# Performance work log

Measured on AMD Instinct MI355X. Metric: run time of the kernel, lower is better.

## Reference

```python
import jax, jax.numpy as jnp
import numpy as np

B, IN, OUT, K = 2048, 1024, 1024, 20


def setup_inputs() -> dict:
    key = jax.random.key(0)
    k1, k2 = jax.random.split(key)
    x = jax.random.normal(k1, (B, IN), dtype=jnp.float32)
    # per-output, per-input spline coefficients: (out_features, in_features, num_knots)
    W = jax.random.normal(k2, (OUT, IN, K), dtype=jnp.float32) * 0.1
    # evenly spaced knot grid on [-2, 2] (linspace)
    knots = jnp.linspace(-2.0, 2.0, K, dtype=jnp.float32)
    return {"x": x, "W": W, "knots": knots}


def reference(x, W, knots):
    # RBF spline basis shared across all output features (this is the fusion
    # the original per-output Python loop misses):
    # basis[b, i, k] = exp(-0.5 * ((x[b, i] - knots[k]) / h)^2)
    h = knots[1] - knots[0]  # uniform knot spacing -> RBF bandwidth
    basis = jnp.exp(-0.5 * jnp.square((x[:, :, None] - knots) / h))  # (B, IN, K)
    # Each SplineLayer o computes sum_{i,k} W[o,i,k] * basis[b,i,k]; the
    # KANBlock concatenates the OUT scalars -> a single einsum.
    return jnp.einsum("bik,oik->bo", basis, W)  # (B, OUT)
```

## Files before the change

### kernel.cpp

```cpp
#include <hip/hip_runtime.h>

#define B_DIM 2048
#define IN_DIM 1024
#define OUT_DIM 1024
#define K_KNOTS 20
#define KR (IN_DIM * K_KNOTS)
#define TM 128
#define TN 128
#define BK 64
#define OUT_ELEMS (B_DIM * OUT_DIM)

#define NB_PAIRS (B_DIM * IN_DIM * K_KNOTS / 2)
#define NB_BASIS_BLK (NB_PAIRS / 256)
#define NW4 (OUT_DIM * KR / 8)
#define NB_W_BLK (NW4 / 256)

typedef __bf16 bf16x8 __attribute__((ext_vector_type(8)));
typedef float  f32x4  __attribute__((ext_vector_type(4)));

__device__ __forceinline__ unsigned short f2bf(float f) {
    unsigned int u = __float_as_uint(f);
    unsigned int r = u + 0x7fffu + ((u >> 16) & 1u);
    return (unsigned short)(r >> 16);
}

__device__ __forceinline__ unsigned int pack2(float lo, float hi) {
    return (unsigned int)f2bf(lo) | ((unsigned int)f2bf(hi) << 16);
}

__device__ __forceinline__ void async_load16(const void* g, void* l) {
    __builtin_amdgcn_global_load_lds(
        (const __attribute__((address_space(1))) void*)g,
        (__attribute__((address_space(3))) void*)l,
        16, 0, 0);
}

__global__ void zero_out_kernel(float* out) {
    int idx = (blockIdx.x * 256 + threadIdx.x) * 4;
    float4 z = {0.f, 0.f, 0.f, 0.f};
    *(float4*)(out + idx) = z;
}

__global__ void prep_kernel(const float* __restrict__ x,
                            const float4* __restrict__ Wsrc,
                            const float* __restrict__ knots,
                            unsigned int* __restrict__ basis_out,
                            uint4* __restrict__ w_out) {
    if (blockIdx.x < NB_BASIS_BLK) {
        unsigned int n = blockIdx.x * 256 + threadIdx.x;
        unsigned int p  = n % 10u;
        unsigned int bi = n / 10u;
        float xv   = x[bi];
        float invh = 1.0f / (knots[1] - knots[0]);
        float t0 = knots[2 * p], t1 = knots[2 * p + 1];
        float d0 = (xv - t0) * invh;
        float d1 = (xv - t1) * invh;
        float v0 = __expf(-0.5f * d0 * d0);
        float v1 = __expf(-0.5f * d1 * d1);
        basis_out[n] = pack2(v0, v1);
    } else {
        unsigned int t = (blockIdx.x - NB_BASIS_BLK) * 256 + threadIdx.x;
        float4 a = Wsrc[2 * t];
        float4 b = Wsrc[2 * t + 1];
        uint4 o;
        o.x = pack2(a.x, a.y);
        o.y = pack2(a.z, a.w);
        o.z = pack2(b.x, b.y);
        o.w = pack2(b.z, b.w);
        w_out[t] = o;
    }
}

template <int KS, bool ATOMIC>
__global__ void __launch_bounds__(256)
kan_gemm(const unsigned short* __restrict__ Ab,
         const unsigned short* __restrict__ Bb,
         float* __restrict__ out) {
    __shared__ __align__(16) unsigned short As[TM * BK];
    __shared__ __align__(16) unsigned short Bs[TN * BK];

    const int KPB = KR / KS;
    const int tid  = threadIdx.x;
    const int wave = tid >> 6;
    const int lane = tid & 63;
    const int wm = wave & 1;
    const int wn = wave >> 1;
    const int m0 = blockIdx.x * TM;
    const int n0 = blockIdx.y * TN;
    const int k0 = blockIdx.z * KPB;

    const int srow = lane >> 3;
    const int scol = ((lane & 7) ^ srow) * 8;

    f32x4 acc[4][4];
#pragma unroll
    for (int i = 0; i < 4; ++i)
#pragma unroll
        for (int j = 0; j < 4; ++j) acc[i][j] = (f32x4){0.f, 0.f, 0.f, 0.f};

    for (int kt = 0; kt < KPB; kt += BK) {
        const int kb = k0 + kt;
        __syncthreads();
#pragma unroll
        for (int c = 0; c < 4; ++c) {
            const int chunk = wave * 4 + c;
            const int r = chunk * 8 + srow;
            async_load16(Ab + (size_t)(m0 + r) * KR + kb + scol, &As[chunk * 512]);
            async_load16(Bb + (size_t)(n0 + r) * KR + kb + scol, &Bs[chunk * 512]);
        }
        __syncthreads();

        const int quad = lane >> 4;
        const int r15  = lane & 15;
        const int r7   = lane & 7;
#pragma unroll
        for (int s = 0; s < 2; ++s) {
            const int cg = s * 4 + quad;
            const int xo = (cg ^ r7) * 8;
            bf16x8 af[4], bfv[4];
#pragma unroll
            for (int i = 0; i < 4; ++i) {
                af[i]  = *(const bf16x8*)&As[(wm * 64 + i * 16 + r15) * BK + xo];
                bfv[i] = *(const bf16x8*)&Bs[(wn * 64 + i * 16 + r15) * BK + xo];
            }
#pragma unroll
            for (int i = 0; i < 4; ++i)
#pragma unroll
                for (int j = 0; j < 4; ++j)
                    acc[i][j] = __builtin_amdgcn_mfma_f32_16x16x32_bf16(
                        af[i], bfv[j], acc[i][j], 0, 0, 0);
        }
    }

    float* dst = ATOMIC ? out : out + (size_t)blockIdx.z * OUT_ELEMS;
    const int quad = lane >> 4;
    const int col  = lane & 15;
#pragma unroll
    for (int i = 0; i < 4; ++i)
#pragma unroll
        for (int j = 0; j < 4; ++j)
#pragma unroll
            for (int r = 0; r < 4; ++r) {
                const int row = m0 + wm * 64 + i * 16 + quad * 4 + r;
                const int c   = n0 + wn * 64 + j * 16 + col;
                if (ATOMIC)
                    atomicAdd(&dst[(size_t)row * OUT_DIM + c], acc[i][j][r]);
                else
                    dst[(size_t)row * OUT_DIM + c] = acc[i][j][r];
            }
}

template <int KS>
__global__ void kan_reduce(const float* __restrict__ part, float* __restrict__ out) {
    const int idx = (blockIdx.x * 256 + threadIdx.x) * 4;
    f32x4 s = *(const f32x4*)(part + idx);
#pragma unroll
    for (int z = 1; z < KS; ++z)
        s += *(const f32x4*)(part + (size_t)z * OUT_ELEMS + idx);
    *(f32x4*)(out + idx) = s;
}

__global__ void kan_fallback(const float* __restrict__ x,
                             const float* __restrict__ W,
                             const float* __restrict__ knots,
                             float* __restrict__ out) {
    __shared__ float basis[256 * K_KNOTS];
    const int b = blockIdx.x;
    const int o = blockIdx.y * blockDim.x + threadIdx.x;
    const float invh = 1.0f / (knots[1] - knots[0]);
    const float* w = W + (size_t)o * KR;
    float sum = 0.f;
    for (int i0 = 0; i0 < IN_DIM; i0 += 256) {
        __syncthreads();
        for (int idx = threadIdx.x; idx < 256 * K_KNOTS; idx += blockDim.x) {
            const int i = i0 + idx / K_KNOTS;
            const int k = idx % K_KNOTS;
            const float d = (x[(size_t)b * IN_DIM + i] - knots[k]) * invh;
            basis[idx] = __expf(-0.5f * d * d);
        }
        __syncthreads();
        for (int r = 0; r < 256 * K_KNOTS; ++r)
            sum += basis[r] * w[(size_t)i0 * K_KNOTS + r];
    }
    out[(size_t)b * OUT_DIM + o] = sum;
}

extern "C" void kernel_launch(void* const* d_in, const int* in_sizes, int n_in,
                              void* d_out, int out_size, void* d_ws, size_t ws_size,
                              hipStream_t stream) {
    const float* x     = (const float*)d_in[0];
    const float* W     = (const float*)d_in[1];
    const float* knots = (const float*)d_in[2];
    float* out = (float*)d_out;

    const size_t basis_bytes = (size_t)B_DIM * KR * 2;
    const size_t wb_bytes    = (size_t)OUT_DIM * KR * 2;
    const size_t part8_bytes = (size_t)8 * OUT_ELEMS * 4;
    const size_t part4_bytes = (size_t)4 * OUT_ELEMS * 4;

    unsigned short* Ab = (unsigned short*)d_ws;
    unsigned short* Bb = (unsigned short*)((char*)d_ws + basis_bytes);
    float* part = (float*)((char*)d_ws + basis_bytes + wb_bytes);

    if (ws_size >= basis_bytes + wb_bytes + part4_bytes) {
        prep_kernel<<<dim3(NB_BASIS_BLK + NB_W_BLK), dim3(256), 0, stream>>>(
            x, (const float4*)W, knots, (unsigned int*)Ab, (uint4*)Bb);
        if (ws_size >= basis_bytes + wb_bytes + part8_bytes) {
            kan_gemm<8, false><<<dim3(B_DIM / TM, OUT_DIM / TN, 8), dim3(256), 0, stream>>>(
                Ab, Bb, part);
            kan_reduce<8><<<dim3(OUT_ELEMS / (256 * 4)), dim3(256), 0, stream>>>(part, out);
        } else {
            kan_gemm<4, false><<<dim3(B_DIM / TM, OUT_DIM / TN, 4), dim3(256), 0, stream>>>(
                Ab, Bb, part);
            kan_reduce<4><<<dim3(OUT_ELEMS / (256 * 4)), dim3(256), 0, stream>>>(part, out);
        }
    } else if (ws_size >= basis_bytes + wb_bytes) {
        zero_out_kernel<<<dim3(OUT_ELEMS / (256 * 4)), dim3(256), 0, stream>>>(out);
        prep_kernel<<<dim3(NB_BASIS_BLK + NB_W_BLK), dim3(256), 0, stream>>>(
            x, (const float4*)W, knots, (unsigned int*)Ab, (uint4*)Bb);
        kan_gemm<4, true><<<dim3(B_DIM / TM, OUT_DIM / TN, 4), dim3(256), 0, stream>>>(
            Ab, Bb, out);
    } else {
        kan_fallback<<<dim3(B_DIM, OUT_DIM / 256), dim3(256), 0, stream>>>(x, W, knots, out);
    }
}
```

Measured before the change: 297.1 us.

## Remap GEMM blocks to XCDs for L2 reuse and fix split-K at four

The GEMM moves to a 1D grid whose block index is decoded so that each of the 8 XCDs (block id mod 8) owns two M-tiles of the basis matrix. Each XCD's L2 then reuses the same A rows across all N tiles and K-splits. The change also drops the 8-way split-K path in favour of a fixed 4-way split. That roughly halves the partial-sum buffer traffic and reduce work, but launches fewer blocks (512 instead of 1024), which may reduce latency hiding.

```diff
diff --git a/kernel.cpp b/kernel.cpp
--- a/kernel.cpp
+++ b/kernel.cpp
@@ -8,7 +8,12 @@
 #define TM 128
 #define TN 128
 #define BK 64
+#define KSPLIT 4
+#define KPB (KR / KSPLIT)
 #define OUT_ELEMS (B_DIM * OUT_DIM)
+#define MT_TILES (B_DIM / TM)
+#define NT_TILES (OUT_DIM / TN)
+#define GEMM_BLOCKS (MT_TILES * NT_TILES * KSPLIT)
 
 #define NB_PAIRS (B_DIM * IN_DIM * K_KNOTS / 2)
 #define NB_BASIS_BLK (NB_PAIRS / 256)
@@ -79,15 +84,22 @@
     __shared__ __align__(16) unsigned short As[TM * BK];
     __shared__ __align__(16) unsigned short Bs[TN * BK];
 
-    const int KPB = KR / KS;
+    const int KPBk = KR / KS;
+    const int id   = blockIdx.x;
+    const int xcd  = id & 7;
+    const int ord  = id >> 3;
+    const int mt   = xcd * 2 + (ord & 1);
+    const int nt   = (ord >> 1) & (NT_TILES - 1);
+    const int z    = ord >> (1 + 3);
+    const int m0 = mt * TM;
+    const int n0 = nt * TN;
+    const int k0 = z * KPBk;
+
     const int tid  = threadIdx.x;
     const int wave = tid >> 6;
     const int lane = tid & 63;
     const int wm = wave & 1;
     const int wn = wave >> 1;
-    const int m0 = blockIdx.x * TM;
-    const int n0 = blockIdx.y * TN;
-    const int k0 = blockIdx.z * KPB;
 
     const int srow = lane >> 3;
     const int scol = ((lane & 7) ^ srow) * 8;
@@ -98,7 +110,7 @@
 #pragma unroll
         for (int j = 0; j < 4; ++j) acc[i][j] = (f32x4){0.f, 0.f, 0.f, 0.f};
 
-    for (int kt = 0; kt < KPB; kt += BK) {
+    for (int kt = 0; kt < KPBk; kt += BK) {
         const int kb = k0 + kt;
         __syncthreads();
 #pragma unroll
@@ -132,7 +144,7 @@
         }
     }
 
-    float* dst = ATOMIC ? out : out + (size_t)blockIdx.z * OUT_ELEMS;
+    float* dst = ATOMIC ? out : out + (size_t)z * OUT_ELEMS;
     const int quad = lane >> 4;
     const int col  = lane & 15;
 #pragma unroll
@@ -195,31 +207,22 @@
 
     const size_t basis_bytes = (size_t)B_DIM * KR * 2;
     const size_t wb_bytes    = (size_t)OUT_DIM * KR * 2;
-    const size_t part8_bytes = (size_t)8 * OUT_ELEMS * 4;
-    const size_t part4_bytes = (size_t)4 * OUT_ELEMS * 4;
+    const size_t part_bytes  = (size_t)KSPLIT * OUT_ELEMS * 4;
 
     unsigned short* Ab = (unsigned short*)d_ws;
     unsigned short* Bb = (unsigned short*)((char*)d_ws + basis_bytes);
     float* part = (float*)((char*)d_ws + basis_bytes + wb_bytes);
 
-    if (ws_size >= basis_bytes + wb_bytes + part4_bytes) {
+    if (ws_size >= basis_bytes + wb_bytes + part_bytes) {
         prep_kernel<<<dim3(NB_BASIS_BLK + NB_W_BLK), dim3(256), 0, stream>>>(
             x, (const float4*)W, knots, (unsigned int*)Ab, (uint4*)Bb);
-        if (ws_size >= basis_bytes + wb_bytes + part8_bytes) {
-            kan_gemm<8, false><<<dim3(B_DIM / TM, OUT_DIM / TN, 8), dim3(256), 0, stream>>>(
-                Ab, Bb, part);
-            kan_reduce<8><<<dim3(OUT_ELEMS / (256 * 4)), dim3(256), 0, stream>>>(part, out);
-        } else {
-            kan_gemm<4, false><<<dim3(B_DIM / TM, OUT_DIM / TN, 4), dim3(256), 0, stream>>>(
-                Ab, Bb, part);
-            kan_reduce<4><<<dim3(OUT_ELEMS / (256 * 4)), dim3(256), 0, stream>>>(part, out);
-        }
+        kan_gemm<KSPLIT, false><<<dim3(GEMM_BLOCKS), dim3(256), 0, stream>>>(Ab, Bb, part);
+        kan_reduce<KSPLIT><<<dim3(OUT_ELEMS / (256 * 4)), dim3(256), 0, stream>>>(part, out);
     } else if (ws_size >= basis_bytes + wb_bytes) {
         zero_out_kernel<<<dim3(OUT_ELEMS / (256 * 4)), dim3(256), 0, stream>>>(out);
         prep_kernel<<<dim3(NB_BASIS_BLK + NB_W_BLK), dim3(256), 0, stream>>>(
             x, (const float4*)W, knots, (unsigned int*)Ab, (uint4*)Bb);
-        kan_gemm<4, true><<<dim3(B_DIM / TM, OUT_DIM / TN, 4), dim3(256), 0, stream>>>(
-            Ab, Bb, out);
+        kan_gemm<KSPLIT, true><<<dim3(GEMM_BLOCKS), dim3(256), 0, stream>>>(Ab, Bb, out);
     } else {
         kan_fallback<<<dim3(B_DIM, OUT_DIM / 256), dim3(256), 0, stream>>>(x, W, knots, out);
     }
```

New measurement: 285.3 us. -4.0%, faster.
